# Optimization experiments

Hardware: AMD Instinct MI355X
Metric: run time of the kernel (lower is better)

Reference implementation:

```python
import jax, jax.numpy as jnp
import numpy as np

DIM = 3; NB = 8; NG = 4; KSIZE = 11; C_IN = 32; C_OUT = 32; HID = 128; NLAYERS = 4
N_PTS = KSIZE ** DIM
EPS = 1e-6

def _build_algebra():
    # Cl(3,0): blades ordered by (grade, bitmask): [1, e1,e2,e3, e12,e13,e23, e123]
    order = sorted(range(NB), key=lambda b: (bin(b).count('1'), b))
    idx = {b: i for i, b in enumerate(order)}
    grades = np.array([bin(b).count('1') for b in order])
    C = np.zeros((NB, NB, NB), np.float32)
    for a in range(NB):
        for b in range(NB):
            s, t = 0, a >> 1
            while t:
                s += bin(t & b).count('1')
                t >>= 1
            C[idx[a], idx[b], idx[a ^ b]] = -1.0 if (s & 1) else 1.0
    paths = np.zeros((NG, NG, NG), bool)
    for i in range(NB):
        for j in range(NB):
            for k in range(NB):
                if C[i, j, k] != 0.0:
                    paths[grades[i], grades[j], grades[k]] = True
    nz = np.argwhere(paths)  # 20 grade-triple paths for Cl(3,0)
    pid = np.zeros((NG, NG, NG), np.int64)
    for p, (a, b, c) in enumerate(nz):
        pid[a, b, c] = p
    pidx = pid[grades[:, None, None], grades[None, :, None], grades[None, None, :]]
    G = np.zeros((NB, NG), np.float32)
    G[np.arange(NB), grades] = 1.0
    return C, pidx, G, len(nz)

_C, _PIDX, _G, N_PATHS = _build_algebra()
CAYLEY = jnp.asarray(_C)   # cayley[a,b,c]: coeff of e_c in e_a * e_b
PIDX = jnp.asarray(_PIDX)  # blade-triple -> grade-path id
GMAT = jnp.asarray(_G)     # (NB, NG) blade->grade one-hot

def grade_norms(x):  # (N,C,NB) -> (N,C,NG)
    return jnp.sqrt(jnp.einsum('ncb,bg->ncg', x * x, GMAT) + EPS)

def to_blades(f):    # (N,C,NG) -> (N,C,NB)
    return jnp.einsum('ncg,bg->ncb', f, GMAT)

def mvlinear(x, w):  # x (N,Ci,NB), w (Co,Ci,NG): grade-wise channel mixing
    wb = jnp.einsum('oig,bg->oib', w, GMAT)
    return jnp.einsum('nib,oib->nob', x, wb)

def mvsilu(x, a, b):  # gated nonlinearity on per-grade invariants
    gate = jax.nn.sigmoid(a * grade_norms(x) + b)
    return x * to_blades(gate)

def gprod(x, q, w):  # per-channel weighted geometric product; w (C, N_PATHS)
    wc = w[:, PIDX] * CAYLEY  # (C, NB, NB, NB) indexed [i,k,j]
    return jnp.einsum('nci,cikj,nck->ncj', x, wc, q)

def _forward(condition, rel_pos_sigma, cond_a, cond_w, cond_b, cayley_weights,
             lin0_w, lin_w, silu_a, silu_b, q_w, gp_w, final_w, shell_sigma):
    lin = jnp.linspace(-1.0, 1.0, KSIZE, dtype=jnp.float32)
    grid = jnp.stack(jnp.meshgrid(lin, lin, lin, indexing='ij'), -1).reshape(-1, DIM)
    rel_pos = grid[:, None, :]                              # (N,1,3)
    norm2 = jnp.sum(rel_pos * rel_pos, -1, keepdims=True)   # (N,1,1)
    scalar = jnp.exp(-norm2 / (2.0 * rel_pos_sigma ** 2))   # scalar shell
    x = jnp.zeros((N_PTS, 1, NB), jnp.float32)
    x = x.at[:, :, 0:1].set(scalar).at[:, :, 1:4].set(rel_pos)  # embed grades 0,1
    relpos_norm = grade_norms(x)[:, 0, :]                   # (N, NG)
    # ConditionGradeNorm: grade-normalize condition, modulated by relpos norms
    cond = jnp.broadcast_to(condition[None], (N_PTS, C_IN, NB))
    gn = grade_norms(cond)
    denom = jax.nn.sigmoid(cond_a) * (gn - 1.0) + 1.0
    scale = (relpos_norm @ cond_w + cond_b).reshape(N_PTS, C_IN, NG)
    cond = cond * to_blades((1.0 + scale) / denom)
    h = jnp.concatenate([x, cond], axis=1)                  # (N, 1+C_IN, NB)
    # KernelNetwork: CEGNN-style MVLinear + MVSiLU + weighted geometric product
    for l in range(NLAYERS):
        h = mvlinear(h, lin0_w if l == 0 else lin_w[l - 1])
        h = mvsilu(h, silu_a[l], silu_b[l])
        h = gprod(h, mvlinear(h, q_w[l]), gp_w[l])
    k = mvlinear(h, final_w).reshape(N_PTS, C_OUT, C_IN, NB)
    # ScalarShell: per (o,i,blade) Gaussian envelope of |rel_pos|^2
    shell = jnp.exp(-norm2 / (2.0 * shell_sigma ** 2)).reshape(N_PTS, C_OUT, C_IN, NB)
    k = k * shell * jnp.float32(1.0 / np.sqrt(N_PTS))       # init factor
    # WeightedCayley: per-(o,i) path weights scattered onto the Cayley table
    wc = jnp.swapaxes(cayley_weights[:, :, PIDX] * CAYLEY, -1, -2)  # (o,i,k,l,m)
    K = jnp.einsum('noik,oiklm->olimn', k, wc)
    return K.reshape(C_OUT * NB, C_IN * NB, KSIZE, KSIZE, KSIZE)

def setup_inputs() -> dict:
    key = jax.random.key(0)
    ks = jax.random.split(key, 10)
    f32 = jnp.float32
    def rn(k, shape, scale=1.0):
        return jax.random.normal(k, shape, f32) * scale
    return {
        'condition': rn(ks[0], (C_IN, NB)),
        'rel_pos_sigma': jnp.ones((1, 1, 1), f32),
        'cond_a': rn(ks[1], (1, C_IN, NG)),
        'cond_w': rn(ks[2], (NG, C_IN * NG), 0.1),
        'cond_b': jnp.zeros((C_IN * NG,), f32),
        'cayley_weights': rn(ks[3], (C_OUT, C_IN, N_PATHS), 1.0 / np.sqrt(C_IN * NB)),
        'lin0_w': rn(ks[4], (HID, 1 + C_IN, NG), 1.0 / np.sqrt(1 + C_IN)),
        'lin_w': rn(ks[5], (NLAYERS - 1, HID, HID, NG), 1.0 / np.sqrt(HID)),
        'silu_a': rn(ks[6], (NLAYERS, 1, HID, NG)),
        'silu_b': jnp.zeros((NLAYERS, 1, HID, NG), f32),
        'q_w': rn(ks[7], (NLAYERS, HID, HID, NG), 1.0 / np.sqrt(HID)),
        'gp_w': rn(ks[8], (NLAYERS, HID, N_PATHS), 0.5),
        'final_w': rn(ks[9], (C_OUT * C_IN, HID, NG), 1.0 / np.sqrt(HID)),
        'shell_sigma': jnp.ones((1, C_OUT * C_IN, NB), f32),
    }

def reference(condition, rel_pos_sigma, cond_a, cond_w, cond_b, cayley_weights,
              lin0_w, lin_w, silu_a, silu_b, q_w, gp_w, final_w, shell_sigma):
    return _forward(condition, rel_pos_sigma, cond_a, cond_w, cond_b, cayley_weights,
                    lin0_w, lin_w, silu_a, silu_b, q_w, gp_w, final_w, shell_sigma)
```

## Files before the change

### kernel.cpp

```cpp
#include <hip/hip_runtime.h>
#include <math.h>

#define NB 8
#define NG 4
#define HID 128
#define NPTS 1331
#define NPAD 1344
#define NT 21
#define EPS 1e-6f

#define LT0_F4   (33*128)
#define MAT_F4   (128*128)
#define ARENA_F4 (LT0_F4 + 7*MAT_F4)

struct Alg {
  int grade[NB];
  signed char gp_j[NB][NB]; float gp_s[NB][NB]; signed char gp_p[NB][NB];
  signed char ks_k[NB][NB]; float ks_s[NB][NB]; signed char ks_p[NB][NB];
};

constexpr int popc3(int x){ return (x&1)+((x>>1)&1)+((x>>2)&1); }

constexpr Alg build_alg(){
  Alg A{};
  int order[NB]{}; int idx[NB]{};
  int t=0;
  for(int g=0; g<=3; ++g) for(int b=0;b<NB;++b) if(popc3(b)==g) order[t++]=b;
  for(int i=0;i<NB;++i) idx[order[i]]=i;
  for(int i=0;i<NB;++i) A.grade[i]=popc3(order[i]);
  float C[NB][NB][NB]{};
  for(int a=0;a<NB;++a) for(int b=0;b<NB;++b){
    int s=0, tt=a>>1;
    while(tt){ s += popc3(tt&b); tt>>=1; }
    C[idx[a]][idx[b]][idx[a^b]] = (s&1)?-1.0f:1.0f;
  }
  bool paths[NG][NG][NG]{};
  for(int i=0;i<NB;++i)for(int j=0;j<NB;++j)for(int k=0;k<NB;++k)
    if(C[i][j][k]!=0.0f) paths[A.grade[i]][A.grade[j]][A.grade[k]]=true;
  int pid[NG][NG][NG]{};
  int p=0;
  for(int a=0;a<NG;++a)for(int b=0;b<NG;++b)for(int c=0;c<NG;++c)
    if(paths[a][b][c]) pid[a][b][c]=p++;
  for(int i=0;i<NB;++i)for(int k=0;k<NB;++k){
    int j = idx[order[i]^order[k]];
    A.gp_j[i][k]=(signed char)j;
    A.gp_s[i][k]=C[i][k][j];
    A.gp_p[i][k]=(signed char)pid[A.grade[i]][A.grade[k]][A.grade[j]];
  }
  for(int l=0;l<NB;++l)for(int m=0;m<NB;++m){
    int k = idx[order[l]^order[m]];
    A.ks_k[l][m]=(signed char)k;
    A.ks_s[l][m]=C[k][m][l];
    A.ks_p[l][m]=(signed char)pid[A.grade[k]][A.grade[m]][A.grade[l]];
  }
  return A;
}

__device__ const Alg ALG = build_alg();

__device__ __forceinline__ float sigm(float x){ return 1.f/(1.f+expf(-x)); }

__global__ __launch_bounds__(256) void k_tw(
    const float4* __restrict__ lin0_w,
    const float4* __restrict__ lin_w,
    const float4* __restrict__ q_w,
    float4* __restrict__ wt)
{
  const int t = blockIdx.x*256 + threadIdx.x;
  if (t >= ARENA_F4) return;
  if (t < LT0_F4){
    const int i = t >> 7, o = t & 127;
    wt[t] = lin0_w[o*33 + i];
  } else {
    const int t2 = t - LT0_F4;
    const int mi = t2 >> 14;
    const int loc = t2 & 16383;
    const int i = loc >> 7, o = loc & 127;
    const float4 v = (mi < 3) ? lin_w[mi*MAT_F4 + o*128 + i]
                              : q_w[(mi-3)*MAT_F4 + o*128 + i];
    wt[t] = v;
  }
}

__global__ __launch_bounds__(256) void k_prep(
    const float* __restrict__ condition,
    const float* __restrict__ sigma1,
    const float* __restrict__ cond_a,
    const float* __restrict__ cond_w,
    const float* __restrict__ cond_b,
    float* __restrict__ norm2_o,
    float* __restrict__ h0)
{
  const int n = blockIdx.x*256 + threadIdx.x;
  if (n >= NPAD) return;
  const bool act = (n < NPTS);
  float px=0.f, py=0.f, pz=0.f, nr=0.f, sc=0.f;
  if (act){
    int i0 = n/121; int r = n - i0*121; int i1 = r/11; int i2 = r - i1*11;
    px = (float)(-1.0 + 0.2*(double)i0);
    py = (float)(-1.0 + 0.2*(double)i1);
    pz = (float)(-1.0 + 0.2*(double)i2);
    nr = px*px + py*py + pz*pz;
    float s = sigma1[0];
    sc = expf(-nr/(2.f*s*s));
  }
  norm2_o[n] = nr;
  h0[(0*HID+0)*NPAD+n] = sc;
  h0[(1*HID+0)*NPAD+n] = px;
  h0[(2*HID+0)*NPAD+n] = py;
  h0[(3*HID+0)*NPAD+n] = pz;
  h0[(4*HID+0)*NPAD+n] = 0.f;
  h0[(5*HID+0)*NPAD+n] = 0.f;
  h0[(6*HID+0)*NPAD+n] = 0.f;
  h0[(7*HID+0)*NPAD+n] = 0.f;
  const float rn0 = sqrtf(sc*sc + EPS);
  const float rn1 = sqrtf(nr + EPS);
  const float rn2 = sqrtf(EPS);
  const float rn3 = sqrtf(EPS);
  for (int c=0;c<32;++c){
    float cb[NB];
    #pragma unroll
    for (int b=0;b<NB;++b) cb[b] = condition[c*8+b];
    float gn2[4];
    gn2[0] = cb[0]*cb[0] + EPS;
    gn2[1] = cb[1]*cb[1] + cb[2]*cb[2] + cb[3]*cb[3] + EPS;
    gn2[2] = cb[4]*cb[4] + cb[5]*cb[5] + cb[6]*cb[6] + EPS;
    gn2[3] = cb[7]*cb[7] + EPS;
    float fac[4];
    #pragma unroll
    for (int g=0; g<4; ++g){
      const float gn = sqrtf(gn2[g]);
      const float den = fmaf(sigm(cond_a[c*4+g]), gn-1.f, 1.f);
      float scl = cond_b[c*4+g];
      scl = fmaf(rn0, cond_w[0*128 + c*4+g], scl);
      scl = fmaf(rn1, cond_w[1*128 + c*4+g], scl);
      scl = fmaf(rn2, cond_w[2*128 + c*4+g], scl);
      scl = fmaf(rn3, cond_w[3*128 + c*4+g], scl);
      fac[g] = (1.f + scl)/den;
    }
    h0[(0*HID + c+1)*NPAD + n] = act ? cb[0]*fac[0] : 0.f;
    h0[(1*HID + c+1)*NPAD + n] = act ? cb[1]*fac[1] : 0.f;
    h0[(2*HID + c+1)*NPAD + n] = act ? cb[2]*fac[1] : 0.f;
    h0[(3*HID + c+1)*NPAD + n] = act ? cb[3]*fac[1] : 0.f;
    h0[(4*HID + c+1)*NPAD + n] = act ? cb[4]*fac[2] : 0.f;
    h0[(5*HID + c+1)*NPAD + n] = act ? cb[5]*fac[2] : 0.f;
    h0[(6*HID + c+1)*NPAD + n] = act ? cb[6]*fac[2] : 0.f;
    h0[(7*HID + c+1)*NPAD + n] = act ? cb[7]*fac[3] : 0.f;
  }
}

template<int KIN>
__device__ __forceinline__ void matvec2(const float* hw, const float4* __restrict__ W,
                                        int c0, int c1, float a0[NB], float a1[NB])
{
  #pragma unroll
  for (int b=0;b<NB;++b){ a0[b]=0.f; a1[b]=0.f; }
  #pragma unroll 4
  for (int i=0;i<KIN;++i){
    const float4 hx = *reinterpret_cast<const float4*>(hw + i*12);
    const float4 hy = *reinterpret_cast<const float4*>(hw + i*12 + 4);
    const float4 w0 = W[i*HID + c0];
    const float4 w1 = W[i*HID + c1];
    a0[0]=fmaf(hx.x,w0.x,a0[0]); a0[1]=fmaf(hx.y,w0.y,a0[1]);
    a0[2]=fmaf(hx.z,w0.y,a0[2]); a0[3]=fmaf(hx.w,w0.y,a0[3]);
    a0[4]=fmaf(hy.x,w0.z,a0[4]); a0[5]=fmaf(hy.y,w0.z,a0[5]);
    a0[6]=fmaf(hy.z,w0.z,a0[6]); a0[7]=fmaf(hy.w,w0.w,a0[7]);
    a1[0]=fmaf(hx.x,w1.x,a1[0]); a1[1]=fmaf(hx.y,w1.y,a1[1]);
    a1[2]=fmaf(hx.z,w1.y,a1[2]); a1[3]=fmaf(hx.w,w1.y,a1[3]);
    a1[4]=fmaf(hy.x,w1.z,a1[4]); a1[5]=fmaf(hy.y,w1.z,a1[5]);
    a1[6]=fmaf(hy.z,w1.z,a1[6]); a1[7]=fmaf(hy.w,w1.w,a1[7]);
  }
}

__device__ __forceinline__ void silu8(float a[NB], const float* sa, const float* sb)
{
  const float g0 = sqrtf(a[0]*a[0] + EPS);
  const float g1 = sqrtf(a[1]*a[1] + a[2]*a[2] + a[3]*a[3] + EPS);
  const float g2 = sqrtf(a[4]*a[4] + a[5]*a[5] + a[6]*a[6] + EPS);
  const float g3 = sqrtf(a[7]*a[7] + EPS);
  const float t0 = sigm(fmaf(sa[0], g0, sb[0]));
  const float t1 = sigm(fmaf(sa[1], g1, sb[1]));
  const float t2 = sigm(fmaf(sa[2], g2, sb[2]));
  const float t3 = sigm(fmaf(sa[3], g3, sb[3]));
  a[0]*=t0; a[1]*=t1; a[2]*=t1; a[3]*=t1; a[4]*=t2; a[5]*=t2; a[6]*=t2; a[7]*=t3;
}

__device__ __forceinline__ void store_row(float* hw, int c, const float a[NB])
{
  float4 v0 = {a[0],a[1],a[2],a[3]};
  float4 v1 = {a[4],a[5],a[6],a[7]};
  *reinterpret_cast<float4*>(hw + c*12)     = v0;
  *reinterpret_cast<float4*>(hw + c*12 + 4) = v1;
}

__device__ __forceinline__ void gprod8(const float x[NB], const float q[NB],
                                       const float wp[20], float o[NB])
{
  #pragma unroll
  for (int b=0;b<NB;++b) o[b]=0.f;
  #pragma unroll
  for (int i=0;i<NB;++i)
    #pragma unroll
    for (int k=0;k<NB;++k){
      const int J = ALG.gp_j[i][k];
      const int P = ALG.gp_p[i][k];
      const float t = x[i]*q[k];
      o[J] = fmaf(ALG.gp_s[i][k] > 0.f ? t : -t, wp[P], o[J]);
    }
}

__global__ __launch_bounds__(512) void k_mlp(
    float* __restrict__ hG,
    const float4* __restrict__ wt,
    const float* __restrict__ silu_a,
    const float* __restrict__ silu_b,
    const float* __restrict__ gp_w)
{
  __shared__ float hl[8][HID][12];
  const int lane = threadIdx.x & 63;
  const int wv   = threadIdx.x >> 6;
  const int n    = blockIdx.x*8 + wv;
  const int c0 = lane, c1 = lane + 64;
  float* hw = &hl[wv][0][0];

  if (lane < 33){
    #pragma unroll
    for (int b=0;b<NB;++b) hw[lane*12+b] = hG[(b*HID+lane)*NPAD + n];
  }

  float a0[NB], a1[NB], q0[NB], q1[NB], o0[NB], o1[NB];
  float wp0[20], wp1[20];

  #pragma unroll 1
  for (int l=0; l<4; ++l){
    const float4* Ql = wt + LT0_F4 + 3*MAT_F4 + (size_t)l*MAT_F4;
    const float* sa = silu_a + l*512;
    const float* sb = silu_b + l*512;
    const float* gw = gp_w  + l*2560;

    if (l == 0) matvec2<33>(hw, wt, c0, c1, a0, a1);
    else        matvec2<HID>(hw, wt + LT0_F4 + (size_t)(l-1)*MAT_F4, c0, c1, a0, a1);
    silu8(a0, sa + c0*4, sb + c0*4);
    silu8(a1, sa + c1*4, sb + c1*4);
    store_row(hw, c0, a0);
    store_row(hw, c1, a1);

    matvec2<HID>(hw, Ql, c0, c1, q0, q1);

    #pragma unroll
    for (int p5=0;p5<5;++p5){
      const float4 v0 = *reinterpret_cast<const float4*>(gw + c0*20 + p5*4);
      const float4 v1 = *reinterpret_cast<const float4*>(gw + c1*20 + p5*4);
      wp0[p5*4+0]=v0.x; wp0[p5*4+1]=v0.y; wp0[p5*4+2]=v0.z; wp0[p5*4+3]=v0.w;
      wp1[p5*4+0]=v1.x; wp1[p5*4+1]=v1.y; wp1[p5*4+2]=v1.z; wp1[p5*4+3]=v1.w;
    }
    gprod8(a0, q0, wp0, o0);
    gprod8(a1, q1, wp1, o1);
    store_row(hw, c0, o0);
    store_row(hw, c1, o1);
  }

  __syncthreads();
  #pragma unroll
  for (int rep=0; rep<16; ++rep){
    const int e  = rep*512 + threadIdx.x;
    const int pt = e & 7;
    const int b  = (e>>3) & 7;
    const int ch = e >> 6;
    hG[(b*HID+ch)*NPAD + blockIdx.x*8 + pt] = hl[pt][ch][b];
  }
}

__global__ __launch_bounds__(256) void k_kfield(
    const float* __restrict__ hin,
    const float* __restrict__ fw,
    const float* __restrict__ ss,
    const float* __restrict__ norm2,
    float* __restrict__ kf)
{
  __shared__ float lds[256*64];
  const int lane = threadIdx.x & 63;
  const int wv   = threadIdx.x >> 6;
  const int nb   = blockIdx.x;
  const int n    = nb*64 + lane;
  const int oi0  = blockIdx.y * 16 + wv * 4;
  float acc[4][NB];
  #pragma unroll
  for (int j=0;j<4;++j)
    #pragma unroll
    for (int b=0;b<NB;++b) acc[j][b]=0.f;

  for (int ci=0; ci<HID; ci+=32){
    __syncthreads();
    #pragma unroll
    for (int rep=0; rep<16; ++rep){
      const int e   = rep*256 + threadIdx.x;
      const int row = e >> 4;
      const int c4  = e & 15;
      const int b   = row >> 5;
      const int cc  = row & 31;
      const float4 v = *reinterpret_cast<const float4*>(hin + (size_t)(b*HID + ci + cc)*NPAD + nb*64 + c4*4);
      *reinterpret_cast<float4*>(&lds[row*64 + c4*4]) = v;
    }
    __syncthreads();
    for (int cc=0; cc<32; ++cc){
      float hv[NB];
      #pragma unroll
      for (int b=0;b<NB;++b) hv[b] = lds[(b*32+cc)*64 + lane];
      #pragma unroll
      for (int j=0;j<4;++j){
        const float4 w = *reinterpret_cast<const float4*>(fw + ((size_t)(oi0+j)*HID + ci+cc)*4);
        acc[j][0] = fmaf(hv[0], w.x, acc[j][0]);
        acc[j][1] = fmaf(hv[1], w.y, acc[j][1]);
        acc[j][2] = fmaf(hv[2], w.y, acc[j][2]);
        acc[j][3] = fmaf(hv[3], w.y, acc[j][3]);
        acc[j][4] = fmaf(hv[4], w.z, acc[j][4]);
        acc[j][5] = fmaf(hv[5], w.z, acc[j][5]);
        acc[j][6] = fmaf(hv[6], w.z, acc[j][6]);
        acc[j][7] = fmaf(hv[7], w.w, acc[j][7]);
      }
    }
  }

  const float INVS = (float)(1.0 / sqrt((double)NPTS));
  const float nr   = norm2[n];
  #pragma unroll
  for (int j=0;j<4;++j){
    const int oi = oi0+j;
    #pragma unroll
    for (int b=0;b<NB;++b){
      const float s = ss[oi*8+b];
      kf[((size_t)oi*8 + b)*NPAD + n] = acc[j][b] * expf(-nr/(2.f*s*s)) * INVS;
    }
  }
}

__global__ __launch_bounds__(256) void k_expand(
    const float* __restrict__ kf,
    const float* __restrict__ cw,
    float* __restrict__ out)
{
  __shared__ float coef[32][8];
  __shared__ int   km[8];
  const int blk = blockIdx.x;
  const int o   = blk >> 6;
  const int l   = (blk >> 3) & 7;
  const int sub = blk & 7;
  const int t   = threadIdx.x;
  {
    const int i = t >> 3, m = t & 7;
    coef[i][m] = ALG.ks_s[l][m] * cw[(size_t)(o*32+i)*20 + ALG.ks_p[l][m]];
    if (t < 8) km[t] = ALG.ks_k[l][t];
  }
  __syncthreads();

  float* obase = out + ((size_t)((o*8+l)*256 + sub*32)) * NPTS;
  #pragma unroll 1
  for (int rr=0; rr<32; ++rr){
    const int row = sub*32 + rr;
    const int i = row >> 3, m = row & 7;
    const float cf = coef[i][m];
    const float* src = kf + ((size_t)((o*32+i)*8 + km[m])) * NPAD;
    float* dst = obase + (size_t)rr * NPTS;
    #pragma unroll
    for (int base=0; base<6; ++base){
      const int idx = base*256 + t;
      if (idx < NPTS) dst[idx] = cf * src[idx];
    }
  }
}

extern "C" void kernel_launch(void* const* d_in, const int* in_sizes, int n_in,
                              void* d_out, int out_size, void* d_ws, size_t ws_size,
                              hipStream_t stream) {
  const float* condition    = (const float*)d_in[0];
  const float* rel_pos_sig  = (const float*)d_in[1];
  const float* cond_a       = (const float*)d_in[2];
  const float* cond_w       = (const float*)d_in[3];
  const float* cond_b       = (const float*)d_in[4];
  const float* cayley_w     = (const float*)d_in[5];
  const float* lin0_w       = (const float*)d_in[6];
  const float* lin_w        = (const float*)d_in[7];
  const float* silu_a       = (const float*)d_in[8];
  const float* silu_b       = (const float*)d_in[9];
  const float* q_w          = (const float*)d_in[10];
  const float* gp_w         = (const float*)d_in[11];
  const float* final_w      = (const float*)d_in[12];
  const float* shell_sigma  = (const float*)d_in[13];
  float* out = (float*)d_out;
  float* ws  = (float*)d_ws;

  float*  norm2 = ws;
  float*  hA    = ws + NPAD;
  float4* arena = (float4*)(hA + 8*HID*NPAD);
  float*  kf    = (float*)(arena + ARENA_F4);

  k_tw<<<dim3((ARENA_F4+255)/256), 256, 0, stream>>>(
      (const float4*)lin0_w, (const float4*)lin_w, (const float4*)q_w, arena);

  k_prep<<<dim3((NPAD+255)/256), 256, 0, stream>>>(
      condition, rel_pos_sig, cond_a, cond_w, cond_b, norm2, hA);

  k_mlp<<<dim3(NPAD/8), 512, 0, stream>>>(hA, arena, silu_a, silu_b, gp_w);

  k_kfield<<<dim3(NT, 64), 256, 0, stream>>>(hA, final_w, shell_sigma, norm2, kf);

  k_expand<<<dim3(2048), 256, 0, stream>>>(kf, cayley_w, out);
}
```

Baseline: 744.6 us.

## Parallelize prep over channels, chunk matvec with barriers, nontemporal expand stores

k_prep now launches a 2D grid with one block row per condition channel instead of looping over 32 channels per thread, giving more parallelism to a small kernel. matvec2 is split into chunks of 16 inputs with a __syncthreads before each chunk, apparently to keep the waves of a block in step for cache and shared-memory reuse of weights, at the cost of extra barriers. The large output writes in k_expand use nontemporal stores to avoid polluting the cache. The added barriers inside matvec2 are only safe if every thread of the block calls it.

```diff
diff --git a/kernel.cpp b/kernel.cpp
--- a/kernel.cpp
+++ b/kernel.cpp
@@ -82,7 +82,7 @@
   }
 }
 
-__global__ __launch_bounds__(256) void k_prep(
+__global__ __launch_bounds__(64) void k_prep(
     const float* __restrict__ condition,
     const float* __restrict__ sigma1,
     const float* __restrict__ cond_a,
@@ -91,8 +91,8 @@
     float* __restrict__ norm2_o,
     float* __restrict__ h0)
 {
-  const int n = blockIdx.x*256 + threadIdx.x;
-  if (n >= NPAD) return;
+  const int n = blockIdx.x*64 + threadIdx.x;
+  const int c = blockIdx.y;
   const bool act = (n < NPTS);
   float px=0.f, py=0.f, pz=0.f, nr=0.f, sc=0.f;
   if (act){
@@ -104,49 +104,51 @@
     float s = sigma1[0];
     sc = expf(-nr/(2.f*s*s));
   }
-  norm2_o[n] = nr;
-  h0[(0*HID+0)*NPAD+n] = sc;
-  h0[(1*HID+0)*NPAD+n] = px;
-  h0[(2*HID+0)*NPAD+n] = py;
-  h0[(3*HID+0)*NPAD+n] = pz;
-  h0[(4*HID+0)*NPAD+n] = 0.f;
-  h0[(5*HID+0)*NPAD+n] = 0.f;
-  h0[(6*HID+0)*NPAD+n] = 0.f;
-  h0[(7*HID+0)*NPAD+n] = 0.f;
+  if (c == 0){
+    norm2_o[n] = nr;
+    h0[(0*HID)*NPAD+n] = sc;
+    h0[(1*HID)*NPAD+n] = px;
+    h0[(2*HID)*NPAD+n] = py;
+    h0[(3*HID)*NPAD+n] = pz;
+    h0[(4*HID)*NPAD+n] = 0.f;
+    h0[(5*HID)*NPAD+n] = 0.f;
+    h0[(6*HID)*NPAD+n] = 0.f;
+    h0[(7*HID)*NPAD+n] = 0.f;
+    return;
+  }
+  const int cc = c-1;
   const float rn0 = sqrtf(sc*sc + EPS);
   const float rn1 = sqrtf(nr + EPS);
   const float rn2 = sqrtf(EPS);
   const float rn3 = sqrtf(EPS);
-  for (int c=0;c<32;++c){
-    float cb[NB];
-    #pragma unroll
-    for (int b=0;b<NB;++b) cb[b] = condition[c*8+b];
-    float gn2[4];
-    gn2[0] = cb[0]*cb[0] + EPS;
-    gn2[1] = cb[1]*cb[1] + cb[2]*cb[2] + cb[3]*cb[3] + EPS;
-    gn2[2] = cb[4]*cb[4] + cb[5]*cb[5] + cb[6]*cb[6] + EPS;
-    gn2[3] = cb[7]*cb[7] + EPS;
-    float fac[4];
-    #pragma unroll
-    for (int g=0; g<4; ++g){
-      const float gn = sqrtf(gn2[g]);
-      const float den = fmaf(sigm(cond_a[c*4+g]), gn-1.f, 1.f);
-      float scl = cond_b[c*4+g];
-      scl = fmaf(rn0, cond_w[0*128 + c*4+g], scl);
-      scl = fmaf(rn1, cond_w[1*128 + c*4+g], scl);
-      scl = fmaf(rn2, cond_w[2*128 + c*4+g], scl);
-      scl = fmaf(rn3, cond_w[3*128 + c*4+g], scl);
-      fac[g] = (1.f + scl)/den;
-    }
-    h0[(0*HID + c+1)*NPAD + n] = act ? cb[0]*fac[0] : 0.f;
-    h0[(1*HID + c+1)*NPAD + n] = act ? cb[1]*fac[1] : 0.f;
-    h0[(2*HID + c+1)*NPAD + n] = act ? cb[2]*fac[1] : 0.f;
-    h0[(3*HID + c+1)*NPAD + n] = act ? cb[3]*fac[1] : 0.f;
-    h0[(4*HID + c+1)*NPAD + n] = act ? cb[4]*fac[2] : 0.f;
-    h0[(5*HID + c+1)*NPAD + n] = act ? cb[5]*fac[2] : 0.f;
-    h0[(6*HID + c+1)*NPAD + n] = act ? cb[6]*fac[2] : 0.f;
-    h0[(7*HID + c+1)*NPAD + n] = act ? cb[7]*fac[3] : 0.f;
-  }
+  float cb[NB];
+  #pragma unroll
+  for (int b=0;b<NB;++b) cb[b] = condition[cc*8+b];
+  float gn2[4];
+  gn2[0] = cb[0]*cb[0] + EPS;
+  gn2[1] = cb[1]*cb[1] + cb[2]*cb[2] + cb[3]*cb[3] + EPS;
+  gn2[2] = cb[4]*cb[4] + cb[5]*cb[5] + cb[6]*cb[6] + EPS;
+  gn2[3] = cb[7]*cb[7] + EPS;
+  float fac[4];
+  #pragma unroll
+  for (int g=0; g<4; ++g){
+    const float gn = sqrtf(gn2[g]);
+    const float den = fmaf(sigm(cond_a[cc*4+g]), gn-1.f, 1.f);
+    float scl = cond_b[cc*4+g];
+    scl = fmaf(rn0, cond_w[0*128 + cc*4+g], scl);
+    scl = fmaf(rn1, cond_w[1*128 + cc*4+g], scl);
+    scl = fmaf(rn2, cond_w[2*128 + cc*4+g], scl);
+    scl = fmaf(rn3, cond_w[3*128 + cc*4+g], scl);
+    fac[g] = (1.f + scl)/den;
+  }
+  h0[(0*HID + c)*NPAD + n] = act ? cb[0]*fac[0] : 0.f;
+  h0[(1*HID + c)*NPAD + n] = act ? cb[1]*fac[1] : 0.f;
+  h0[(2*HID + c)*NPAD + n] = act ? cb[2]*fac[1] : 0.f;
+  h0[(3*HID + c)*NPAD + n] = act ? cb[3]*fac[1] : 0.f;
+  h0[(4*HID + c)*NPAD + n] = act ? cb[4]*fac[2] : 0.f;
+  h0[(5*HID + c)*NPAD + n] = act ? cb[5]*fac[2] : 0.f;
+  h0[(6*HID + c)*NPAD + n] = act ? cb[6]*fac[2] : 0.f;
+  h0[(7*HID + c)*NPAD + n] = act ? cb[7]*fac[3] : 0.f;
 }
 
 template<int KIN>
@@ -155,20 +157,27 @@
 {
   #pragma unroll
   for (int b=0;b<NB;++b){ a0[b]=0.f; a1[b]=0.f; }
-  #pragma unroll 4
-  for (int i=0;i<KIN;++i){
-    const float4 hx = *reinterpret_cast<const float4*>(hw + i*12);
-    const float4 hy = *reinterpret_cast<const float4*>(hw + i*12 + 4);
-    const float4 w0 = W[i*HID + c0];
-    const float4 w1 = W[i*HID + c1];
-    a0[0]=fmaf(hx.x,w0.x,a0[0]); a0[1]=fmaf(hx.y,w0.y,a0[1]);
-    a0[2]=fmaf(hx.z,w0.y,a0[2]); a0[3]=fmaf(hx.w,w0.y,a0[3]);
-    a0[4]=fmaf(hy.x,w0.z,a0[4]); a0[5]=fmaf(hy.y,w0.z,a0[5]);
-    a0[6]=fmaf(hy.z,w0.z,a0[6]); a0[7]=fmaf(hy.w,w0.w,a0[7]);
-    a1[0]=fmaf(hx.x,w1.x,a1[0]); a1[1]=fmaf(hx.y,w1.y,a1[1]);
-    a1[2]=fmaf(hx.z,w1.y,a1[2]); a1[3]=fmaf(hx.w,w1.y,a1[3]);
-    a1[4]=fmaf(hy.x,w1.z,a1[4]); a1[5]=fmaf(hy.y,w1.z,a1[5]);
-    a1[6]=fmaf(hy.z,w1.z,a1[6]); a1[7]=fmaf(hy.w,w1.w,a1[7]);
+  #pragma unroll
+  for (int i0=0; i0<KIN; i0+=16){
+    __syncthreads();
+    const int lim = (KIN - i0 < 16) ? (KIN - i0) : 16;
+    #pragma unroll
+    for (int ii=0; ii<16; ++ii){
+      if (ii >= lim) break;
+      const int i = i0 + ii;
+      const float4 hx = *reinterpret_cast<const float4*>(hw + i*12);
+      const float4 hy = *reinterpret_cast<const float4*>(hw + i*12 + 4);
+      const float4 w0 = W[i*HID + c0];
+      const float4 w1 = W[i*HID + c1];
+      a0[0]=fmaf(hx.x,w0.x,a0[0]); a0[1]=fmaf(hx.y,w0.y,a0[1]);
+      a0[2]=fmaf(hx.z,w0.y,a0[2]); a0[3]=fmaf(hx.w,w0.y,a0[3]);
+      a0[4]=fmaf(hy.x,w0.z,a0[4]); a0[5]=fmaf(hy.y,w0.z,a0[5]);
+      a0[6]=fmaf(hy.z,w0.z,a0[6]); a0[7]=fmaf(hy.w,w0.w,a0[7]);
+      a1[0]=fmaf(hx.x,w1.x,a1[0]); a1[1]=fmaf(hx.y,w1.y,a1[1]);
+      a1[2]=fmaf(hx.z,w1.y,a1[2]); a1[3]=fmaf(hx.w,w1.y,a1[3]);
+      a1[4]=fmaf(hy.x,w1.z,a1[4]); a1[5]=fmaf(hy.y,w1.z,a1[5]);
+      a1[6]=fmaf(hy.z,w1.z,a1[6]); a1[7]=fmaf(hy.w,w1.w,a1[7]);
+    }
   }
 }
 
@@ -365,7 +374,7 @@
     #pragma unroll
     for (int base=0; base<6; ++base){
       const int idx = base*256 + t;
-      if (idx < NPTS) dst[idx] = cf * src[idx];
+      if (idx < NPTS) __builtin_nontemporal_store(cf * src[idx], &dst[idx]);
     }
   }
 }
@@ -398,7 +407,7 @@
   k_tw<<<dim3((ARENA_F4+255)/256), 256, 0, stream>>>(
       (const float4*)lin0_w, (const float4*)lin_w, (const float4*)q_w, arena);
 
-  k_prep<<<dim3((NPAD+255)/256), 256, 0, stream>>>(
+  k_prep<<<dim3(NT, 33), 64, 0, stream>>>(
       condition, rel_pos_sig, cond_a, cond_w, cond_b, norm2, hA);
 
   k_mlp<<<dim3(NPAD/8), 512, 0, stream>>>(hA, arena, silu_a, silu_b, gp_w);
```

Measured after the change: 780.4 us. 1.05x slower.
